# Kernel tuning notes

Hardware: AMD Instinct MI355X
Metric: run time of the kernel (lower is better)

Reference implementation:

```python
import jax, jax.numpy as jnp
import numpy as np

B, S, E, H = 4, 2048, 1024, 16
DH = E // H
EXP = 1024  # FeedForwardPart default expansion_dim
EPS = 1e-5


def layer_norm(x, gamma, beta):
    mu = jnp.mean(x, axis=-1, keepdims=True)
    var = jnp.var(x, axis=-1, keepdims=True)
    return (x - mu) * jax.lax.rsqrt(var + EPS) * gamma + beta


def setup_inputs() -> dict:
    key = jax.random.key(0)
    ks = jax.random.split(key, 8)
    s = 0.02
    return {
        "x": jax.random.normal(ks[0], (B, S, E), jnp.float32),
        "mask": jnp.ones((B, 1, 1, S), jnp.int32),
        "wq": jax.random.normal(ks[1], (E, E), jnp.float32) * s,
        "wk": jax.random.normal(ks[2], (E, E), jnp.float32) * s,
        "wv": jax.random.normal(ks[3], (E, E), jnp.float32) * s,
        "wo": jax.random.normal(ks[4], (E, E), jnp.float32) * s,
        "bo": jnp.zeros((E,), jnp.float32),
        "w1": jax.random.normal(ks[5], (E, EXP), jnp.float32) * s,
        "b1": jnp.zeros((EXP,), jnp.float32),
        "w2": jax.random.normal(ks[6], (EXP, E), jnp.float32) * s,
        "b2": jnp.zeros((E,), jnp.float32),
        "gamma": jnp.ones((E,), jnp.float32),
        "beta": jnp.zeros((E,), jnp.float32),
    }


def reference(x, mask, wq, wk, wv, wo, bo, w1, b1, w2, b2, gamma, beta):
    # Multi-head self-attention
    q = (x @ wq).reshape(B, S, H, DH)
    k = (x @ wk).reshape(B, S, H, DH)
    v = (x @ wv).reshape(B, S, H, DH)
    scores = jnp.einsum("bqhd,bkhd->bhqk", q, k) / jnp.sqrt(jnp.float32(DH))
    scores = jnp.where(mask == 0, jnp.float32(-1e10), scores)
    attn = jax.nn.softmax(scores, axis=-1)
    ctx = jnp.einsum("bhqk,bkhd->bqhd", attn, v).reshape(B, S, E)
    attn_out = ctx @ wo + bo
    # Residual + shared LayerNorm
    h = layer_norm(attn_out + x, gamma, beta)
    # FFN (expansion 1024 per source default)
    ff = jax.nn.relu(h @ w1 + b1) @ w2 + b2
    return layer_norm(ff + h, gamma, beta)
```

## Files before the change

kernel.cpp:

```cpp
#include <hip/hip_runtime.h>
#include <hip/hip_bf16.h>

typedef short s16x8 __attribute__((ext_vector_type(8)));
typedef float f32x4 __attribute__((ext_vector_type(4)));
typedef float f32x16 __attribute__((ext_vector_type(16)));
typedef unsigned short u16;

#define B_ 4
#define S_ 2048
#define E_ 1024
#define H_ 16
#define DH_ 64

__device__ __forceinline__ u16 f2b(float f) {
  union { float f; unsigned u; } x; x.f = f;
  unsigned r = (x.u + 0x7fffu + ((x.u >> 16) & 1u)) >> 16;
  return (u16)r;
}

__device__ __forceinline__ float b2f(u16 v) {
  union { unsigned u; float f; } x; x.u = ((unsigned)v) << 16; return x.f;
}

__device__ __forceinline__ unsigned pk2(float lo, float hi) {
  __hip_bfloat162 h = __float22bfloat162_rn(float2{lo, hi});
  union { __hip_bfloat162 h; unsigned u; } c; c.h = h; return c.u;
}

__device__ __forceinline__ float fexp2(float x) { return __builtin_amdgcn_exp2f(x); }

__device__ __forceinline__ void pl32swap(unsigned& x, unsigned& y) {
  asm("v_permlane32_swap_b32 %0, %1" : "+v"(x), "+v"(y));
}

__device__ __forceinline__ void async16(const void* g, void* l) {
  __builtin_amdgcn_global_load_lds((const __attribute__((address_space(1))) void*)g,
                                   (__attribute__((address_space(3))) void*)l,
                                   16, 0, 0);
}

__global__ __launch_bounds__(256) void k_cast(const float* __restrict__ in,
                                              u16* __restrict__ out, int n4) {
  int i = blockIdx.x * 256 + threadIdx.x;
  if (i >= n4) return;
  float4 v = ((const float4*)in)[i];
  ushort4 o;
  o.x = f2b(v.x); o.y = f2b(v.y); o.z = f2b(v.z); o.w = f2b(v.w);
  ((ushort4*)out)[i] = o;
}

__global__ __launch_bounds__(256) void k_castT(const float* __restrict__ in,
                                               u16* __restrict__ out, int K, int N) {
  __shared__ float tile[32][33];
  int k0 = blockIdx.x * 32, n0 = blockIdx.y * 32;
  int tx = threadIdx.x, ty = threadIdx.y;
#pragma unroll
  for (int i = 0; i < 32; i += 8)
    tile[ty + i][tx] = in[(long)(k0 + ty + i) * N + n0 + tx];
  __syncthreads();
#pragma unroll
  for (int i = 0; i < 32; i += 8)
    out[(long)(n0 + ty + i) * K + k0 + tx] = f2b(tile[tx][ty + i]);
}

__global__ __launch_bounds__(256, 2) void k_gemm(
    const u16* __restrict__ A, const u16* __restrict__ Bt,
    int N, int K,
    const float* __restrict__ bias, int relu, int mode,
    float* __restrict__ outF, u16* __restrict__ outB,
    u16* __restrict__ oq, u16* __restrict__ ok, u16* __restrict__ ov) {
  __shared__ __align__(16) u16 Al[128 * 32];
  __shared__ __align__(16) u16 Bl[128 * 32];
  const int t = threadIdx.x;
  const int lane = t & 63, w = t >> 6;
  const int g = lane >> 4, li = lane & 15;
  const int wr = w >> 1, wc = w & 1;
  const int bm = blockIdx.x * 128, bn = blockIdx.y * 128;

  f32x4 acc[4][4] = {};

  const long ar0 = bm + (t >> 2), ar1 = bm + ((256 + t) >> 2);
  const long br0 = bn + (t >> 2), br1 = bn + ((256 + t) >> 2);
  const int c0 = (t & 3) * 8, c1 = ((256 + t) & 3) * 8;
  u16* aD0 = &Al[(w * 64) * 8];
  u16* aD1 = &Al[(256 + w * 64) * 8];
  u16* bD0 = &Bl[(w * 64) * 8];
  u16* bD1 = &Bl[(256 + w * 64) * 8];

  for (int kt = 0; kt < K; kt += 32) {
    async16(&A[ar0 * K + kt + c0], aD0);
    async16(&A[ar1 * K + kt + c1], aD1);
    async16(&Bt[br0 * K + kt + c0], bD0);
    async16(&Bt[br1 * K + kt + c1], bD1);
    __syncthreads();
    s16x8 af[4], bf[4];
#pragma unroll
    for (int mi = 0; mi < 4; ++mi)
      af[mi] = *(const s16x8*)&Al[(wr * 64 + mi * 16 + li) * 32 + g * 8];
#pragma unroll
    for (int nf = 0; nf < 4; ++nf)
      bf[nf] = *(const s16x8*)&Bl[(wc * 64 + nf * 16 + li) * 32 + g * 8];
#pragma unroll
    for (int mi = 0; mi < 4; ++mi)
#pragma unroll
      for (int nf = 0; nf < 4; ++nf)
        acc[mi][nf] = __builtin_amdgcn_mfma_f32_16x16x32_bf16(af[mi], bf[nf], acc[mi][nf], 0, 0, 0);
    __syncthreads();
  }

#pragma unroll
  for (int mi = 0; mi < 4; ++mi)
#pragma unroll
    for (int nf = 0; nf < 4; ++nf) {
      int col = bn + wc * 64 + nf * 16 + li;
      if (mode == 1) {
        int which = col >> 10, cc = col & 1023;
        int hh = cc >> 6, dd = cc & 63;
        u16* dst = which == 0 ? oq : (which == 1 ? ok : ov);
        float scl = which == 0 ? 0.18033688011112042f : 1.f;
#pragma unroll
        for (int r = 0; r < 4; ++r) {
          long row = bm + wr * 64 + mi * 16 + g * 4 + r;
          int b2 = (int)(row >> 11), ss = (int)(row & 2047);
          dst[(((long)b2 * H_ + hh) * S_ + ss) * DH_ + dd] = f2b(acc[mi][nf][r] * scl);
        }
      } else {
        float bv = bias ? bias[col] : 0.f;
#pragma unroll
        for (int r = 0; r < 4; ++r) {
          long row = bm + wr * 64 + mi * 16 + g * 4 + r;
          float v = acc[mi][nf][r] + bv;
          if (relu) v = fmaxf(v, 0.f);
          if (outF) outF[row * N + col] = v;
          if (outB) outB[row * N + col] = f2b(v);
        }
      }
    }
}

__global__ __launch_bounds__(512) void k_attn(
    const u16* __restrict__ Q, const u16* __restrict__ Kg, const u16* __restrict__ Vg,
    const int* __restrict__ mask, u16* __restrict__ ctx) {
  __shared__ __align__(16) u16 Kl[3][64 * 64];
  __shared__ __align__(16) u16 Vt[3][64 * 72];
  __shared__ __align__(16) float MBs[S_];
  __shared__ int MFlag[S_ / 64];
  __shared__ __align__(16) float BC[8 * 32];
  const int t = threadIdx.x;
  const int lane = t & 63, wid = t >> 6;
  const int q = lane & 31, hi = lane >> 5;
  const int bh = blockIdx.x;
  const int b = bh >> 4, h = bh & 15;
  const long bhoff = (long)bh * S_ * DH_;
  const int q0 = blockIdx.y * 256 + wid * 32;
  const int skey = t >> 3, sdj = t & 7;
  const int NT = S_ / 64;

  {
    int4 m4 = ((const int4*)(mask + (long)b * S_))[t];
    float4 f;
    f.x = m4.x ? 0.f : -1e10f; f.y = m4.y ? 0.f : -1e10f;
    f.z = m4.z ? 0.f : -1e10f; f.w = m4.w ? 0.f : -1e10f;
    ((float4*)MBs)[t] = f;
    bool ok = m4.x && m4.y && m4.z && m4.w;
    unsigned long long vote = __ballot(ok);
    if ((lane & 15) == 0)
      MFlag[t >> 4] = (((vote >> ((lane >> 4) * 16)) & 0xFFFFull) == 0xFFFFull);
  }

  s16x8 qf[4];
  {
    const u16* Qp = Q + bhoff + (long)(q0 + q) * DH_;
#pragma unroll
    for (int c = 0; c < 4; ++c) qf[c] = *(const s16x8*)(Qp + c * 16 + hi * 8);
  }

  s16x8 kreg, vreg;
#define LOADKV(TI) { \
    kreg = *(const s16x8*)(Kg + bhoff + (long)((TI) * 64 + skey) * DH_ + sdj * 8); \
    vreg = *(const s16x8*)(Vg + bhoff + (long)((TI) * 64 + lane) * DH_ + wid * 8); }
#define WRITEKV(BUF) { \
    *(s16x8*)((char*)&Kl[BUF][0] + skey * 128 + ((sdj * 16) ^ ((skey & 7) << 4))) = kreg; \
    _Pragma("unroll") \
    for (int j = 0; j < 8; ++j) Vt[BUF][(wid * 8 + j) * 72 + lane] = (u16)vreg[j]; }

  const int swz = (q & 7) << 4;
#define QKSTEP(S0, S1, BUF) { \
    const char* Kc = (const char*)&Kl[BUF][0]; \
    _Pragma("unroll") \
    for (int c = 0; c < 4; ++c) { \
      s16x8 kf0 = *(const s16x8*)(Kc + q * 128 + ((c * 32 + hi * 16) ^ swz)); \
      s16x8 kf1 = *(const s16x8*)(Kc + (32 + q) * 128 + ((c * 32 + hi * 16) ^ swz)); \
      S0 = __builtin_amdgcn_mfma_f32_32x32x16_bf16(kf0, qf[c], S0, 0, 0, 0); \
      S1 = __builtin_amdgcn_mfma_f32_32x32x16_bf16(kf1, qf[c], S1, 0, 0, 0); \
    } }

#define SOFTPV(S0, S1, TI) { \
    const int kt = (TI) * 64; \
    const u16* Vc = &Vt[(TI) % 3][0]; \
    const bool mok = MFlag[TI] != 0; \
    float p[32]; \
    float t00 = -1e30f, t01 = -1e30f, t10 = -1e30f, t11 = -1e30f; \
    if (mok) { \
      _Pragma("unroll") \
      for (int j = 0; j < 16; j += 2) { \
        p[j] = S0[j]; p[j + 1] = S0[j + 1]; \
        p[16 + j] = S1[j]; p[16 + j + 1] = S1[j + 1]; \
        t00 = fmaxf(t00, S0[j]); t01 = fmaxf(t01, S0[j + 1]); \
        t10 = fmaxf(t10, S1[j]); t11 = fmaxf(t11, S1[j + 1]); \
      } \
    } else { \
      _Pragma("unroll") \
      for (int g4 = 0; g4 < 4; ++g4) { \
        f32x4 mb0 = *(const f32x4*)&MBs[kt + g4 * 8 + hi * 4]; \
        f32x4 mb1 = *(const f32x4*)&MBs[kt + 32 + g4 * 8 + hi * 4]; \
        _Pragma("unroll") \
        for (int e = 0; e < 4; ++e) { \
          float v0 = S0[g4 * 4 + e] + mb0[e]; \
          float v1 = S1[g4 * 4 + e] + mb1[e]; \
          p[g4 * 4 + e] = v0; p[16 + g4 * 4 + e] = v1; \
          if (e & 1) { t01 = fmaxf(t01, v0); t11 = fmaxf(t11, v1); } \
          else       { t00 = fmaxf(t00, v0); t10 = fmaxf(t10, v1); } \
        } \
      } \
    } \
    float tmax = fmaxf(fmaxf(t00, t01), fmaxf(t10, t11)); \
    tmax = fmaxf(tmax, __shfl_xor(tmax, 32)); \
    if (!__all(tmax <= m_run + 11.5f)) { \
      float mnew = fmaxf(m_run, tmax); \
      float corr = fexp2(m_run - mnew); \
      m_run = mnew; l_run *= corr; \
      if (lane < 32) BC[wid * 32 + q] = corr; \
      asm volatile("s_waitcnt lgkmcnt(0)" ::: "memory"); \
      _Pragma("unroll") \
      for (int g4 = 0; g4 < 4; ++g4) { \
        f32x4 cv = *(const f32x4*)&BC[wid * 32 + g4 * 8 + hi * 4]; \
        _Pragma("unroll") \
        for (int e = 0; e < 4; ++e) { o0[g4 * 4 + e] *= cv[e]; o1[g4 * 4 + e] *= cv[e]; } \
      } \
    } \
    float ps0 = 0.f, ps1 = 0.f, ps2 = 0.f, ps3 = 0.f; \
    _Pragma("unroll") \
    for (int j = 0; j < 32; j += 4) { \
      float a = fexp2(p[j] - m_run), b2v = fexp2(p[j + 1] - m_run); \
      float c = fexp2(p[j + 2] - m_run), d = fexp2(p[j + 3] - m_run); \
      p[j] = a; p[j + 1] = b2v; p[j + 2] = c; p[j + 3] = d; \
      ps0 += a; ps1 += b2v; ps2 += c; ps3 += d; \
    } \
    l_run += (ps0 + ps1) + (ps2 + ps3); \
    _Pragma("unroll") \
    for (int c = 0; c < 4; ++c) { \
      unsigned X1 = pk2(p[c * 8 + 0], p[c * 8 + 1]); \
      unsigned X2 = pk2(p[c * 8 + 2], p[c * 8 + 3]); \
      unsigned Y1 = pk2(p[c * 8 + 4], p[c * 8 + 5]); \
      unsigned Y2 = pk2(p[c * 8 + 6], p[c * 8 + 7]); \
      pl32swap(X1, Y1); pl32swap(X2, Y2); \
      union { unsigned u[4]; s16x8 v; } pu; \
      pu.u[0] = X1; pu.u[1] = X2; pu.u[2] = Y1; pu.u[3] = Y2; \
      s16x8 vb0 = *(const s16x8*)(Vc + (long)q * 72 + c * 16 + hi * 8); \
      s16x8 vb1 = *(const s16x8*)(Vc + (long)(32 + q) * 72 + c * 16 + hi * 8); \
      o0 = __builtin_amdgcn_mfma_f32_32x32x16_bf16(pu.v, vb0, o0, 0, 0, 0); \
      o1 = __builtin_amdgcn_mfma_f32_32x32x16_bf16(pu.v, vb1, o1, 0, 0, 0); \
    } }

#define ITER(I, SC0, SC1, SN0, SN1) { \
    const int ip1 = (I) + 1; \
    if (ip1 < NT) WRITEKV(ip1 % 3); \
    __syncthreads(); \
    if (ip1 < NT) { \
      SN0 = zz; SN1 = zz; \
      QKSTEP(SN0, SN1, ip1 % 3); \
      if (ip1 + 1 < NT) LOADKV(ip1 + 1); \
    } \
    SOFTPV(SC0, SC1, I); }

  f32x16 zz = {};
  f32x16 o0 = zz, o1 = zz;
  float m_run = -1e30f, l_run = 0.f;

  LOADKV(0);
  WRITEKV(0);
  __syncthreads();
  f32x16 sA0 = zz, sA1 = zz, sB0 = zz, sB1 = zz;
  QKSTEP(sA0, sA1, 0);
  LOADKV(1);

  for (int i = 0; i < NT; i += 2) {
    ITER(i, sA0, sA1, sB0, sB1);
    ITER(i + 1, sB0, sB1, sA0, sA1);
  }

  l_run += __shfl_xor(l_run, 32);
  float inv = 1.f / fmaxf(l_run, 1e-30f);
  if (lane < 32) BC[wid * 32 + q] = inv;
  asm volatile("s_waitcnt lgkmcnt(0)" ::: "memory");
#pragma unroll
  for (int g4 = 0; g4 < 4; ++g4) {
    f32x4 iv = *(const f32x4*)&BC[wid * 32 + g4 * 8 + hi * 4];
#pragma unroll
    for (int e = 0; e < 4; ++e) {
      int qr = e + g4 * 8 + hi * 4;
      long ro = ((long)(b * S_ + q0 + qr) * H_ + h) * DH_ + q;
      ctx[ro] = f2b(o0[g4 * 4 + e] * iv[e]);
      ctx[ro + 32] = f2b(o1[g4 * 4 + e] * iv[e]);
    }
  }
#undef LOADKV
#undef WRITEKV
#undef QKSTEP
#undef SOFTPV
#undef ITER
}

__global__ __launch_bounds__(256) void k_lnb(const u16* __restrict__ a, const u16* __restrict__ res,
                                             const float* __restrict__ gamma, const float* __restrict__ beta,
                                             float* __restrict__ outF, u16* __restrict__ outB) {
  const int row = blockIdx.x, t = threadIdx.x;
  const long base = (long)row * E_;
  ushort4 av = ((const ushort4*)(a + base))[t];
  ushort4 rv = ((const ushort4*)(res + base))[t];
  float4 s = make_float4(b2f(av.x) + b2f(rv.x), b2f(av.y) + b2f(rv.y),
                         b2f(av.z) + b2f(rv.z), b2f(av.w) + b2f(rv.w));
  float ps = s.x + s.y + s.z + s.w;
  float pq = s.x * s.x + s.y * s.y + s.z * s.z + s.w * s.w;
#pragma unroll
  for (int xm = 32; xm >= 1; xm >>= 1) { ps += __shfl_xor(ps, xm); pq += __shfl_xor(pq, xm); }
  __shared__ float red[8];
  int w = t >> 6, lane = t & 63;
  if (lane == 0) { red[w] = ps; red[4 + w] = pq; }
  __syncthreads();
  ps = red[0] + red[1] + red[2] + red[3];
  pq = red[4] + red[5] + red[6] + red[7];
  float mu = ps * (1.f / E_);
  float rs = rsqrtf(pq * (1.f / E_) - mu * mu + 1e-5f);
  float4 gv = ((const float4*)gamma)[t];
  float4 be = ((const float4*)beta)[t];
  float4 o = make_float4((s.x - mu) * rs * gv.x + be.x, (s.y - mu) * rs * gv.y + be.y,
                         (s.z - mu) * rs * gv.z + be.z, (s.w - mu) * rs * gv.w + be.w);
  if (outF) ((float4*)(outF + base))[t] = o;
  if (outB) {
    ushort4 ob; ob.x = f2b(o.x); ob.y = f2b(o.y); ob.z = f2b(o.z); ob.w = f2b(o.w);
    ((ushort4*)(outB + base))[t] = ob;
  }
}

extern "C" void kernel_launch(void* const* d_in, const int* in_sizes, int n_in,
                              void* d_out, int out_size, void* d_ws, size_t ws_size,
                              hipStream_t stream) {
  const float* x  = (const float*)d_in[0];
  const int* mask = (const int*)d_in[1];
  const float* wq = (const float*)d_in[2];
  const float* wk = (const float*)d_in[3];
  const float* wv = (const float*)d_in[4];
  const float* wo = (const float*)d_in[5];
  const float* bo = (const float*)d_in[6];
  const float* w1 = (const float*)d_in[7];
  const float* b1 = (const float*)d_in[8];
  const float* w2 = (const float*)d_in[9];
  const float* b2 = (const float*)d_in[10];
  const float* gamma = (const float*)d_in[11];
  const float* beta  = (const float*)d_in[12];
  float* out = (float*)d_out;

  char* ws = (char*)d_ws;
  const size_t MB = 1024ull * 1024ull;
  u16* xb  = (u16*)(ws + 0);
  u16* wqt = (u16*)(ws + 16 * MB);
  u16* wkt = (u16*)(ws + 18 * MB);
  u16* wvt = (u16*)(ws + 20 * MB);
  u16* wot = (u16*)(ws + 22 * MB);
  u16* w1t = (u16*)(ws + 24 * MB);
  u16* w2t = (u16*)(ws + 26 * MB);
  u16* qb  = (u16*)(ws + 28 * MB);
  u16* kb  = (u16*)(ws + 44 * MB);
  u16* vb  = (u16*)(ws + 60 * MB);
  u16* ctx = (u16*)(ws + 76 * MB);
  u16* aob = (u16*)(ws + 92 * MB);
  u16* hb  = (u16*)(ws + 108 * MB);
  u16* ff1 = qb;
  u16* ff2b = kb;

  const int n4 = B_ * S_ * E_ / 4;
  k_cast<<<n4 / 256, 256, 0, stream>>>(x, xb, n4);
  dim3 tg(E_ / 32, E_ / 32), tb(32, 8);
  k_castT<<<tg, tb, 0, stream>>>(wq, wqt, E_, E_);
  k_castT<<<tg, tb, 0, stream>>>(wk, wkt, E_, E_);
  k_castT<<<tg, tb, 0, stream>>>(wv, wvt, E_, E_);
  k_castT<<<tg, tb, 0, stream>>>(wo, wot, E_, E_);
  k_castT<<<tg, tb, 0, stream>>>(w1, w1t, E_, E_);
  k_castT<<<tg, tb, 0, stream>>>(w2, w2t, E_, E_);

  k_gemm<<<dim3(64, 24), 256, 0, stream>>>(xb, wqt, 3072, 1024, nullptr, 0, 1,
                                           nullptr, nullptr, qb, kb, vb);

  k_attn<<<dim3(B_ * H_, S_ / 256), 512, 0, stream>>>(qb, kb, vb, mask, ctx);

  dim3 gg(64, 8);
  k_gemm<<<gg, 256, 0, stream>>>(ctx, wot, 1024, 1024, bo, 0, 0, nullptr, aob,
                                 nullptr, nullptr, nullptr);
  k_lnb<<<B_ * S_, 256, 0, stream>>>(aob, xb, gamma, beta, nullptr, hb);
  k_gemm<<<gg, 256, 0, stream>>>(hb, w1t, 1024, 1024, b1, 1, 0, nullptr, ff1,
                                 nullptr, nullptr, nullptr);
  k_gemm<<<gg, 256, 0, stream>>>(ff1, w2t, 1024, 1024, b2, 0, 0, nullptr, ff2b,
                                 nullptr, nullptr, nullptr);
  k_lnb<<<B_ * S_, 256, 0, stream>>>(ff2b, hb, gamma, beta, out, nullptr);
}
```

Baseline: 313.4 us.

## Add dedicated 256x256 pipelined QKV projection GEMM kernel

Replaces the generic 128x128 GEMM for the fused QKV projection with a new 256x256-tile kernel using 512 threads. It double-buffers K-slices in LDS through async global-to-LDS copies, uses an XOR-swizzled LDS layout, and interleaves staging with MFMA phases under explicit barriers and priority hints. A block-index swizzle is added for L2 locality. This targets the load/compute stalls and low data reuse of the smaller-tile kernel, at the cost of higher register and LDS use (one block per CU) and fragile hand-scheduled waitcnts.

Measured after the change: 324.6 us. +3.6%, slower.

```diff
diff --git a/kernel.cpp b/kernel.cpp
--- a/kernel.cpp
+++ b/kernel.cpp
@@ -66,9 +66,8 @@
 __global__ __launch_bounds__(256, 2) void k_gemm(
     const u16* __restrict__ A, const u16* __restrict__ Bt,
     int N, int K,
-    const float* __restrict__ bias, int relu, int mode,
-    float* __restrict__ outF, u16* __restrict__ outB,
-    u16* __restrict__ oq, u16* __restrict__ ok, u16* __restrict__ ov) {
+    const float* __restrict__ bias, int relu,
+    float* __restrict__ outF, u16* __restrict__ outB) {
   __shared__ __align__(16) u16 Al[128 * 32];
   __shared__ __align__(16) u16 Bl[128 * 32];
   const int t = threadIdx.x;
@@ -113,29 +112,128 @@
 #pragma unroll
     for (int nf = 0; nf < 4; ++nf) {
       int col = bn + wc * 64 + nf * 16 + li;
-      if (mode == 1) {
-        int which = col >> 10, cc = col & 1023;
-        int hh = cc >> 6, dd = cc & 63;
-        u16* dst = which == 0 ? oq : (which == 1 ? ok : ov);
-        float scl = which == 0 ? 0.18033688011112042f : 1.f;
-#pragma unroll
-        for (int r = 0; r < 4; ++r) {
-          long row = bm + wr * 64 + mi * 16 + g * 4 + r;
-          int b2 = (int)(row >> 11), ss = (int)(row & 2047);
-          dst[(((long)b2 * H_ + hh) * S_ + ss) * DH_ + dd] = f2b(acc[mi][nf][r] * scl);
-        }
-      } else {
-        float bv = bias ? bias[col] : 0.f;
-#pragma unroll
-        for (int r = 0; r < 4; ++r) {
-          long row = bm + wr * 64 + mi * 16 + g * 4 + r;
-          float v = acc[mi][nf][r] + bv;
-          if (relu) v = fmaxf(v, 0.f);
-          if (outF) outF[row * N + col] = v;
-          if (outB) outB[row * N + col] = f2b(v);
-        }
+      float bv = bias ? bias[col] : 0.f;
+#pragma unroll
+      for (int r = 0; r < 4; ++r) {
+        long row = bm + wr * 64 + mi * 16 + g * 4 + r;
+        float v = acc[mi][nf][r] + bv;
+        if (relu) v = fmaxf(v, 0.f);
+        if (outF) outF[row * N + col] = v;
+        if (outB) outB[row * N + col] = f2b(v);
       }
     }
+}
+
+__global__ __launch_bounds__(512, 1) void k_qkv256(
+    const u16* __restrict__ A, const u16* __restrict__ Bt,
+    u16* __restrict__ oq, u16* __restrict__ ok, u16* __restrict__ ov) {
+  __shared__ __align__(16) u16 Al[2][256 * 64];
+  __shared__ __align__(16) u16 Bl[2][256 * 64];
+  const int t = threadIdx.x, lane = t & 63, w = t >> 6;
+  const int li = lane & 15, g = lane >> 4;
+  const int wr = w >> 2, wc = w & 3;
+  const int swzb = (blockIdx.x & 7) * 48 + (blockIdx.x >> 3);
+  const int bm = (swzb & 31) * 256;
+  const int bn = (swzb >> 5) * 256;
+  const int srl = lane >> 3;
+  const int scc = ((lane & 7) ^ srl) * 8;
+
+  f32x4 acc[8][4] = {};
+  s16x8 aR[4][2], bR[2][2][2];
+
+#define STG_A(BUF, H, C, TK) { \
+    const int rb = (w >> 2) * 128 + (H) * 64 + ((w & 3) + 4 * (C)) * 8; \
+    async16(A + (long)(bm + rb + srl) * 1024 + (TK) * 64 + scc, &Al[BUF][rb * 64]); }
+#define STG_B(BUF, NH, C, TK) { \
+    const int rb = (w >> 1) * 64 + (NH) * 32 + ((w & 1) + 2 * (C)) * 8; \
+    async16(Bt + (long)(bn + rb + srl) * 1024 + (TK) * 64 + scc, &Bl[BUF][rb * 64]); }
+#define STG_AH(BUF, H, TK)  { STG_A(BUF, H, 0, TK); STG_A(BUF, H, 1, TK); }
+#define STG_BNH(BUF, NH, TK) { STG_B(BUF, NH, 0, TK); STG_B(BUF, NH, 1, TK); }
+
+#define RD_A(BUF, MH) { \
+    _Pragma("unroll") for (int f = 0; f < 4; ++f) { \
+      const int row = wr * 128 + (MH) * 64 + f * 16 + li; \
+      _Pragma("unroll") for (int s = 0; s < 2; ++s) \
+        aR[f][s] = *(const s16x8*)&Al[BUF][row * 64 + (((s * 4 + g) ^ (li & 7)) << 3)]; } }
+#define RD_B(BUF, NH) { \
+    _Pragma("unroll") for (int n = 0; n < 2; ++n) { \
+      const int row = wc * 64 + (NH) * 32 + n * 16 + li; \
+      _Pragma("unroll") for (int s = 0; s < 2; ++s) \
+        bR[NH][n][s] = *(const s16x8*)&Bl[BUF][row * 64 + (((s * 4 + g) ^ (li & 7)) << 3)]; } }
+
+#define MFMA16(MH, NH) { \
+    _Pragma("unroll") for (int f = 0; f < 4; ++f) \
+    _Pragma("unroll") for (int n = 0; n < 2; ++n) \
+    _Pragma("unroll") for (int s = 0; s < 2; ++s) \
+      acc[(MH) * 4 + f][(NH) * 2 + n] = __builtin_amdgcn_mfma_f32_16x16x32_bf16( \
+          aR[f][s], bR[NH][n][s], acc[(MH) * 4 + f][(NH) * 2 + n], 0, 0, 0); }
+
+#define XBAR { __builtin_amdgcn_sched_barrier(0); __builtin_amdgcn_s_barrier(); }
+#define SP1 __builtin_amdgcn_s_setprio(1)
+#define SP0 __builtin_amdgcn_s_setprio(0)
+
+  STG_AH(0, 0, 0); STG_BNH(0, 0, 0); STG_AH(0, 1, 0); STG_BNH(0, 1, 0);
+  STG_AH(1, 0, 1); STG_BNH(1, 0, 1); STG_AH(1, 1, 1);
+  asm volatile("s_waitcnt vmcnt(6)" ::: "memory");
+  XBAR;
+
+  for (int it = 0; it < 8; ++it) {
+    const int tp1 = (it * 2 + 1) & 15, tp2 = (it * 2 + 2) & 15, tp3 = (it * 2 + 3) & 15;
+    RD_A(0, 0); RD_B(0, 0);
+    STG_BNH(1, 1, tp1);
+    XBAR; SP1; MFMA16(0, 0); SP0; XBAR;
+    RD_B(0, 1);
+    STG_AH(0, 0, tp2);
+    XBAR; SP1; MFMA16(0, 1); SP0; XBAR;
+    RD_A(0, 1);
+    STG_BNH(0, 0, tp2);
+    XBAR; SP1; MFMA16(1, 1); SP0; XBAR;
+    STG_AH(0, 1, tp2);
+    XBAR; SP1; MFMA16(1, 0); SP0;
+    asm volatile("s_waitcnt vmcnt(6)" ::: "memory");
+    XBAR;
+    RD_A(1, 0); RD_B(1, 0);
+    STG_BNH(0, 1, tp2);
+    XBAR; SP1; MFMA16(0, 0); SP0; XBAR;
+    RD_B(1, 1);
+    STG_AH(1, 0, tp3);
+    XBAR; SP1; MFMA16(0, 1); SP0; XBAR;
+    RD_A(1, 1);
+    STG_BNH(1, 0, tp3);
+    XBAR; SP1; MFMA16(1, 1); SP0; XBAR;
+    STG_AH(1, 1, tp3);
+    XBAR; SP1; MFMA16(1, 0); SP0;
+    asm volatile("s_waitcnt vmcnt(6)" ::: "memory");
+    XBAR;
+  }
+  asm volatile("s_waitcnt vmcnt(0)" ::: "memory");
+
+#pragma unroll
+  for (int f = 0; f < 8; ++f)
+#pragma unroll
+    for (int n = 0; n < 4; ++n) {
+      int col = bn + wc * 64 + n * 16 + li;
+      int which = col >> 10, cc = col & 1023;
+      int hh = cc >> 6, dd = cc & 63;
+      u16* dst = which == 0 ? oq : (which == 1 ? ok : ov);
+      float scl = which == 0 ? 0.18033688011112042f : 1.f;
+#pragma unroll
+      for (int r = 0; r < 4; ++r) {
+        long row = bm + wr * 128 + f * 16 + g * 4 + r;
+        int b2 = (int)(row >> 11), ss = (int)(row & 2047);
+        dst[(((long)b2 * H_ + hh) * S_ + ss) * DH_ + dd] = f2b(acc[f][n][r] * scl);
+      }
+    }
+#undef STG_A
+#undef STG_B
+#undef STG_AH
+#undef STG_BNH
+#undef RD_A
+#undef RD_B
+#undef MFMA16
+#undef XBAR
+#undef SP1
+#undef SP0
 }
 
 __global__ __launch_bounds__(512) void k_attn(
@@ -390,18 +488,14 @@
   k_castT<<<tg, tb, 0, stream>>>(w1, w1t, E_, E_);
   k_castT<<<tg, tb, 0, stream>>>(w2, w2t, E_, E_);
 
-  k_gemm<<<dim3(64, 24), 256, 0, stream>>>(xb, wqt, 3072, 1024, nullptr, 0, 1,
-                                           nullptr, nullptr, qb, kb, vb);
+  k_qkv256<<<384, 512, 0, stream>>>(xb, wqt, qb, kb, vb);
 
   k_attn<<<dim3(B_ * H_, S_ / 256), 512, 0, stream>>>(qb, kb, vb, mask, ctx);
 
   dim3 gg(64, 8);
-  k_gemm<<<gg, 256, 0, stream>>>(ctx, wot, 1024, 1024, bo, 0, 0, nullptr, aob,
-                                 nullptr, nullptr, nullptr);
+  k_gemm<<<gg, 256, 0, stream>>>(ctx, wot, 1024, 1024, bo, 0, nullptr, aob);
   k_lnb<<<B_ * S_, 256, 0, stream>>>(aob, xb, gamma, beta, nullptr, hb);
-  k_gemm<<<gg, 256, 0, stream>>>(hb, w1t, 1024, 1024, b1, 1, 0, nullptr, ff1,
-                                 nullptr, nullptr, nullptr);
-  k_gemm<<<gg, 256, 0, stream>>>(ff1, w2t, 1024, 1024, b2, 0, 0, nullptr, ff2b,
-                                 nullptr, nullptr, nullptr);
+  k_gemm<<<gg, 256, 0, stream>>>(hb, w1t, 1024, 1024, b1, 1, nullptr, ff1);
+  k_gemm<<<gg, 256, 0, stream>>>(ff1, w2t, 1024, 1024, b2, 0, nullptr, ff2b);
   k_lnb<<<B_ * S_, 256, 0, stream>>>(ff2b, hb, gamma, beta, out, nullptr);
 }
```
